# Kernel optimization log

Measured on AMD Instinct MI355X. Metric: run time of the kernel, lower is better.

Reference implementation:

```python
import jax, jax.numpy as jnp
import numpy as np

B, S, D = 2, 2048, 2048
H, DH = 16, 128  # heads, dhead


def setup_inputs() -> dict:
    key = jax.random.key(0)
    k1, k2, k3 = jax.random.split(key, 3)
    x = jax.random.normal(k1, (B, S, D), dtype=jnp.float32)
    # torch Linear weights: [out_features, in_features], fan_in-scaled init
    w_in = jax.random.normal(k2, (3 * H * DH, D), dtype=jnp.float32) * (1.0 / np.sqrt(D))
    w_out = jax.random.normal(k3, (D, H * DH), dtype=jnp.float32) * (1.0 / np.sqrt(H * DH))
    return {"x": x, "w_in": w_in, "w_out": w_out}


def reference(x, w_in, w_out):
    b, s, _ = x.shape
    # input projection (no bias): [b, s, 3*H*DH]
    projected = jnp.einsum("bsd,ed->bse", x, w_in)
    # view(b, s, H, 3*DH) then chunk along last dim -> q, k, v each [b, s, H, DH]
    projected = projected.reshape(b, s, H, 3 * DH)
    q, k, v = jnp.split(projected, 3, axis=-1)
    # naive path: scores [b, H, s, s]
    scores = jnp.einsum("bqhd,bkhd->bhqk", q, k) * (1.0 / np.sqrt(DH))
    # causal mask (tril keeps, upper triangle -> -inf)
    causal_mask = jnp.tril(jnp.ones((s, s), dtype=bool))
    scores = jnp.where(causal_mask, scores, jnp.float32(-jnp.inf))
    attn = jax.nn.softmax(scores, axis=-1)
    # PV: [b, s, H, DH]
    out = jnp.einsum("bhqk,bkhd->bqhd", attn, v)
    out = out.reshape(b, s, H * DH)
    # output projection (no bias): [b, s, D]
    return jnp.einsum("bse,de->bsd", out, w_out)
```

## Files before the change

kernel.cpp:

```cpp
#include <hip/hip_runtime.h>
#include <hip/hip_bf16.h>
#include <math.h>


typedef short bf16x8 __attribute__((ext_vector_type(8)));
typedef float f32x4 __attribute__((ext_vector_type(4)));

#define NEG_BIG -30000.0f

__device__ __forceinline__ short f2bf(float f) {
    union { float f; unsigned u; } v; v.f = f;
    unsigned r = v.u + 0x7fffu + ((v.u >> 16) & 1u);
    return (short)(r >> 16);
}

__device__ __forceinline__ int pack2bf(float a, float b) {
    return (int)((((unsigned)f2bf(b)) << 16) | (((unsigned)f2bf(a)) & 0xffffu));
}

#define GLDS16(g, l) \
    __builtin_amdgcn_global_load_lds((const __attribute__((address_space(1))) void*)(g), \
                                     (__attribute__((address_space(3))) void*)(l), 16, 0, 0)

__global__ __launch_bounds__(256) void cvt_f32_bf16(const float* __restrict__ src,
                                                    short* __restrict__ dst, int n) {
    int i = (blockIdx.x * blockDim.x + threadIdx.x) * 4;
    if (i < n) {
        float4 v = *(const float4*)(src + i);
        short4 o;
        o.x = f2bf(v.x); o.y = f2bf(v.y); o.z = f2bf(v.z); o.w = f2bf(v.w);
        *(short4*)(dst + i) = o;
    }
}

template <int BN, bool F32OUT>
__global__ __launch_bounds__(256) void gemm_bt(const short* __restrict__ A,
                                               const short* __restrict__ Bm,
                                               void* __restrict__ Cv,
                                               int N, int K) {
    constexpr int NT = BN / 32;
    constexpr int SUBA = 128 * 32;
    constexpr int SUBB = BN * 32;
    __shared__ short sA[2 * SUBA];
    __shared__ short sB[2 * SUBB];
    const int lane = threadIdx.x & 63;
    const int w = threadIdx.x >> 6;
    const int l15 = lane & 15, quad = lane >> 4;
    const int bm0 = blockIdx.y * 128, bn0 = blockIdx.x * BN;

    const int c1 = w * 64 + lane;
    const short* gA = A + (size_t)(bm0 + (c1 >> 2)) * K + (c1 & 3) * 8;
    const short* gB = Bm + (size_t)(bn0 + (c1 >> 2)) * K + (c1 & 3) * 8;
    const size_t half64 = (size_t)64 * K;
    short* lA1 = sA + w * 512;
    short* lA2 = sA + 2048 + w * 512;
    short* lB1 = sB + w * 512;
    short* lB2 = sB + 2048 + w * 512;

    const int wm = (w >> 1) * 64, wn = (w & 1) * (BN / 2);
    const short* pa = sA + (wm + l15) * 32 + quad * 8;
    const short* pb = sB + (wn + l15) * 32 + quad * 8;

    f32x4 acc[4][NT] = {};
    for (int k0 = 0; k0 < K; k0 += 64) {
        #pragma unroll
        for (int s = 0; s < 2; s++) {
            const int ks = k0 + s * 32;
            GLDS16(gA + ks, lA1 + s * SUBA);
            GLDS16(gA + half64 + ks, lA2 + s * SUBA);
            GLDS16(gB + ks, lB1 + s * SUBB);
            if constexpr (BN == 128) GLDS16(gB + half64 + ks, lB2 + s * SUBB);
        }
        __syncthreads();
        #pragma unroll
        for (int s = 0; s < 2; s++) {
            bf16x8 af[4], bf[NT];
            #pragma unroll
            for (int mt = 0; mt < 4; mt++) af[mt] = *(const bf16x8*)(pa + s * SUBA + mt * 512);
            #pragma unroll
            for (int nt = 0; nt < NT; nt++) bf[nt] = *(const bf16x8*)(pb + s * SUBB + nt * 512);
            #pragma unroll
            for (int mt = 0; mt < 4; mt++)
                #pragma unroll
                for (int nt = 0; nt < NT; nt++)
                    acc[mt][nt] = __builtin_amdgcn_mfma_f32_16x16x32_bf16(af[mt], bf[nt], acc[mt][nt], 0, 0, 0);
        }
        __syncthreads();
    }
    #pragma unroll
    for (int mt = 0; mt < 4; mt++)
        #pragma unroll
        for (int nt = 0; nt < NT; nt++)
            #pragma unroll
            for (int r = 0; r < 4; r++) {
                int row = bm0 + wm + mt * 16 + quad * 4 + r;
                int col = bn0 + wn + nt * 16 + l15;
                if (F32OUT)
                    ((float*)Cv)[(size_t)row * N + col] = acc[mt][nt][r];
                else
                    ((short*)Cv)[(size_t)row * N + col] = f2bf(acc[mt][nt][r]);
            }
}

#define VP 40
__global__ __launch_bounds__(512) void attn_kernel(const short* __restrict__ P,
                                                   short* __restrict__ O) {
    constexpr int S = 2048, ROWW = 6144, HD = 2048;
    const int id = blockIdx.x;
    const int b = id >> 8;
    const int rr = id & 255;
    const int h = rr & 15;
    const int t0 = rr >> 4;
    const int qt = b ? (15 - t0) : t0;
    const int wave = threadIdx.x >> 6, lane = threadIdx.x & 63;
    const int l15 = lane & 15, quad = lane >> 4;
    const int qRow = qt * 128 + wave * 16;
    const short* Pb = P + (size_t)b * S * ROWW;
    const short* Qp = Pb + h * 384;
    const short* Kp = Qp + 128;
    const short* Vp = Qp + 256;

    __shared__ short sK[2][32 * 128];
    __shared__ short sVt[2][128 * VP];

    bf16x8 qf[4];
    #pragma unroll
    for (int f = 0; f < 4; f++)
        qf[f] = *(const bf16x8*)(Qp + (size_t)(qRow + l15) * ROWW + f * 32 + quad * 8);

    const bool isK = wave < 4;
    const int c1 = (wave & 3) * 64 + lane;
    const int krow1 = c1 >> 4;
    const int kcol = ((c1 & 15) ^ (krow1 & 15)) * 8;
    const short* gK1 = Kp + (size_t)krow1 * ROWW + kcol;
    const short* gK2 = Kp + (size_t)(krow1 + 16) * ROWW + kcol;
    const int ldsOff1 = (wave & 3) * 512;
    const int ldsOff2 = 2048 + (wave & 3) * 512;
    const int vt = (int)threadIdx.x - 256;
    const int vKey = vt & 31;
    const int vD0 = (vt >> 5) * 8;
    const short* gV = Vp + (size_t)vKey * ROWW + vD0;

    const int kTiles = qt * 4 + 4;
    const float scale = 0.08838834764831845f;
    const int qG = qRow + l15;

    f32x4 accO[8] = {};
    float m_i = NEG_BIG, l_i = 0.f;

    if (isK) {
        GLDS16(gK1, &sK[0][ldsOff1]);
        GLDS16(gK2, &sK[0][ldsOff2]);
    } else {
        bf16x8 v0 = *(const bf16x8*)(gV);
        bf16x8 v1 = *(const bf16x8*)(gV + 64);
        #pragma unroll
        for (int j = 0; j < 8; j++) {
            sVt[0][(vD0 + j) * VP + vKey] = v0[j];
            sVt[0][(vD0 + 64 + j) * VP + vKey] = v1[j];
        }
    }
    __syncthreads();

    for (int kt = 0; kt < kTiles; kt++) {
        const int cur = kt & 1, nxt = cur ^ 1;
        const bool pre = (kt + 1 < kTiles);
        bf16x8 v0n, v1n;
        if (pre) {
            const size_t kOff = (size_t)(kt + 1) * 32 * ROWW;
            if (isK) {
                GLDS16(gK1 + kOff, &sK[nxt][ldsOff1]);
                GLDS16(gK2 + kOff, &sK[nxt][ldsOff2]);
            } else {
                v0n = *(const bf16x8*)(gV + kOff);
                v1n = *(const bf16x8*)(gV + kOff + 64);
            }
        }
        f32x4 sc[2] = {};
        #pragma unroll
        for (int hh = 0; hh < 2; hh++) {
            const int row = hh * 16 + l15;
            #pragma unroll
            for (int f = 0; f < 4; f++) {
                const int jj = (4 * f + quad) ^ l15;
                bf16x8 kf = *(const bf16x8*)(&sK[cur][row * 128 + jj * 8]);
                sc[hh] = __builtin_amdgcn_mfma_f32_16x16x32_bf16(kf, qf[f], sc[hh], 0, 0, 0);
            }
        }
        #pragma unroll
        for (int hh = 0; hh < 2; hh++)
            #pragma unroll
            for (int r = 0; r < 4; r++) {
                int key = kt * 32 + hh * 16 + quad * 4 + r;
                float v = sc[hh][r] * scale;
                sc[hh][r] = (key <= qG) ? v : NEG_BIG;
            }
        float mloc = sc[0][0];
        #pragma unroll
        for (int r = 1; r < 4; r++) mloc = fmaxf(mloc, sc[0][r]);
        #pragma unroll
        for (int r = 0; r < 4; r++) mloc = fmaxf(mloc, sc[1][r]);
        mloc = fmaxf(mloc, __shfl_xor(mloc, 16));
        mloc = fmaxf(mloc, __shfl_xor(mloc, 32));
        const float nm = fmaxf(m_i, mloc);
        const float alpha = __expf(m_i - nm);
        m_i = nm;
        float ssum = 0.f;
        #pragma unroll
        for (int hh = 0; hh < 2; hh++)
            #pragma unroll
            for (int r = 0; r < 4; r++) {
                float p = __expf(sc[hh][r] - nm);
                sc[hh][r] = p;
                ssum += p;
            }
        ssum += __shfl_xor(ssum, 16);
        ssum += __shfl_xor(ssum, 32);
        l_i = alpha * l_i + ssum;
        #pragma unroll
        for (int t = 0; t < 8; t++)
            #pragma unroll
            for (int r = 0; r < 4; r++) accO[t][r] *= alpha;
        const int d00 = pack2bf(sc[0][0], sc[0][1]);
        const int d01 = pack2bf(sc[0][2], sc[0][3]);
        const int d10 = pack2bf(sc[1][0], sc[1][1]);
        const int d11 = pack2bf(sc[1][2], sc[1][3]);
        const int srcA = l15 + ((quad & 1) << 5);
        const int srcB = srcA + 16;
        const int s00 = __shfl(d00, srcA), s01 = __shfl(d01, srcA);
        const int s02 = __shfl(d00, srcB), s03 = __shfl(d01, srcB);
        const int s10 = __shfl(d10, srcA), s11 = __shfl(d11, srcA);
        const int s12 = __shfl(d10, srcB), s13 = __shfl(d11, srcB);
        union { int i[4]; bf16x8 v; } pu;
        const bool lo = quad < 2;
        pu.i[0] = lo ? s00 : s10;
        pu.i[1] = lo ? s01 : s11;
        pu.i[2] = lo ? s02 : s12;
        pu.i[3] = lo ? s03 : s13;
        const bf16x8 pf = pu.v;
        #pragma unroll
        for (int t = 0; t < 8; t++) {
            bf16x8 vf = *(const bf16x8*)(&sVt[cur][(t * 16 + l15) * VP + quad * 8]);
            accO[t] = __builtin_amdgcn_mfma_f32_16x16x32_bf16(vf, pf, accO[t], 0, 0, 0);
        }
        if (pre && !isK) {
            #pragma unroll
            for (int j = 0; j < 8; j++) {
                sVt[nxt][(vD0 + j) * VP + vKey] = v0n[j];
                sVt[nxt][(vD0 + 64 + j) * VP + vKey] = v1n[j];
            }
        }
        __syncthreads();
    }
    const float inv = 1.0f / l_i;
    #pragma unroll
    for (int t = 0; t < 8; t++) {
        short4 st;
        st.x = f2bf(accO[t][0] * inv);
        st.y = f2bf(accO[t][1] * inv);
        st.z = f2bf(accO[t][2] * inv);
        st.w = f2bf(accO[t][3] * inv);
        *(short4*)(&O[(size_t)(b * S + qG) * HD + h * 128 + t * 16 + quad * 4]) = st;
    }
}

extern "C" void kernel_launch(void* const* d_in, const int* in_sizes, int n_in,
                              void* d_out, int out_size, void* d_ws, size_t ws_size,
                              hipStream_t stream) {
    const float* x     = (const float*)d_in[0];
    const float* w_in  = (const float*)d_in[1];
    const float* w_out = (const float*)d_in[2];
    float* out = (float*)d_out;

    short* Pbuf   = (short*)d_ws;
    short* xObuf  = Pbuf  + (size_t)4096 * 6144;
    short* winb   = xObuf + (size_t)8388608;
    short* woutb  = winb  + (size_t)6144 * 2048;

    dim3 blk(256, 1, 1);
    const int nx = 2 * 2048 * 2048, nwi = 6144 * 2048, nwo = 2048 * 2048;
    hipLaunchKernelGGL(cvt_f32_bf16, dim3(nx / 1024), blk, 0, stream, x, xObuf, nx);
    hipLaunchKernelGGL(cvt_f32_bf16, dim3(nwi / 1024), blk, 0, stream, w_in, winb, nwi);
    hipLaunchKernelGGL(cvt_f32_bf16, dim3(nwo / 1024), blk, 0, stream, w_out, woutb, nwo);
    hipLaunchKernelGGL((gemm_bt<128, false>), dim3(48, 32, 1), blk, 0, stream, xObuf, winb, (void*)Pbuf, 6144, 2048);
    hipLaunchKernelGGL(attn_kernel, dim3(512, 1, 1), dim3(512, 1, 1), 0, stream, Pbuf, xObuf);
    hipLaunchKernelGGL((gemm_bt<64, true>), dim3(32, 32, 1), blk, 0, stream, xObuf, woutb, (void*)out, 2048, 2048);
}
```

Before: 387.0 us.

## Replace input-projection GEMM with 256x256-tile double-buffered pipelined kernel

Adds a new GEMM kernel with 256x256 output tiles, 512 threads and 8 waves. It uses XOR-swizzled LDS layouts, direct global-to-LDS loads and a phased prefetch schedule that interleaves loads with MFMA work, plus blockIdx swizzling for cache locality. The kernel is used for the QKV input projection. The aim is higher data reuse per tile and better overlap of memory traffic with compute. The cost is heavy register and LDS use (128 KB of shared memory) and a hand-tuned wait/barrier schedule that is fragile.

```diff
diff --git a/kernel.cpp b/kernel.cpp
--- a/kernel.cpp
+++ b/kernel.cpp
@@ -96,6 +96,134 @@
                 int row = bm0 + wm + mt * 16 + quad * 4 + r;
                 int col = bn0 + wn + nt * 16 + l15;
                 if (F32OUT)
+                    ((float*)Cv)[(size_t)row * N + col] = acc[mt][nt][r];
+                else
+                    ((short*)Cv)[(size_t)row * N + col] = f2bf(acc[mt][nt][r]);
+            }
+}
+
+struct MainT { static constexpr bool value = false; };
+struct TailT { static constexpr bool value = true; };
+
+template <bool F32OUT>
+__global__ __launch_bounds__(512, 2) void gemm256(const short* __restrict__ A,
+                                                  const short* __restrict__ Bm,
+                                                  void* __restrict__ Cv,
+                                                  int N, int K, int MT) {
+    __shared__ short sA[2][256 * 64];
+    __shared__ short sB[2][256 * 64];
+    const int tid = threadIdx.x;
+    const int lane = tid & 63, w = tid >> 6;
+    const int l15 = lane & 15, quad = lane >> 4;
+    const int wm = w >> 2, wn = w & 3;
+
+    const int cpx = (int)gridDim.x >> 3;
+    const int swz = ((int)blockIdx.x & 7) * cpx + ((int)blockIdx.x >> 3);
+    const int bm0 = (swz % MT) * 256;
+    const int bn0 = (swz / MT) * 256;
+
+    const int rloc = w * 8 + (lane >> 3);
+    const int csw = ((lane & 7) ^ ((lane >> 3) & 7)) * 8;
+    const short* gA = A + (size_t)(bm0 + rloc) * K + csw;
+    const short* gB = Bm + (size_t)(bn0 + rloc) * K + csw;
+
+    auto stA = [&](int buf, int R0, int t) {
+        GLDS16(gA + (size_t)R0 * K + t * 64, &sA[buf][R0 * 64 + w * 512]);
+    };
+    auto stB = [&](int buf, int R0, int t) {
+        GLDS16(gB + (size_t)R0 * K + t * 64, &sB[buf][R0 * 64 + w * 512]);
+    };
+
+    const int sx = l15 & 7;
+    auto ldA = [&](int buf, int r0, int ks) -> bf16x8 {
+        const int off = (r0 + l15) * 128 + (((ks * 4 + quad) ^ sx) << 4);
+        return *(const bf16x8*)((const char*)&sA[buf][0] + off);
+    };
+    auto ldB = [&](int buf, int r0, int ks) -> bf16x8 {
+        const int off = (r0 + l15) * 128 + (((ks * 4 + quad) ^ sx) << 4);
+        return *(const bf16x8*)((const char*)&sB[buf][0] + off);
+    };
+
+    f32x4 acc[8][4] = {};
+    bf16x8 bfr[4][2];
+
+    stB(0, 0, 0); stB(0, 64, 0); stB(0, 128, 0); stB(0, 192, 0);
+    stA(0, 0, 0); stA(0, 128, 0); stA(0, 64, 0); stA(0, 192, 0);
+    stB(1, 0, 1); stB(1, 64, 1); stB(1, 128, 1); stB(1, 192, 1);
+    stA(1, 0, 1); stA(1, 128, 1);
+    asm volatile("s_waitcnt vmcnt(6)" ::: "memory");
+    __builtin_amdgcn_s_barrier();
+
+    auto iter = [&](auto TC, int t0) {
+        constexpr bool TAIL = decltype(TC)::value;
+        #pragma unroll
+        for (int tt = 0; tt < 2; ++tt) {
+            const int buf = tt;
+            #pragma unroll
+            for (int q = 0; q < 4; ++q) {
+                const int ph = tt * 4 + q;
+                bf16x8 afr[2][2];
+                if (q == 0) {
+                    #pragma unroll
+                    for (int nt = 0; nt < 4; ++nt)
+                        #pragma unroll
+                        for (int ks = 0; ks < 2; ++ks)
+                            bfr[nt][ks] = ldB(buf, wn * 64 + nt * 16, ks);
+                }
+                #pragma unroll
+                for (int mt = 0; mt < 2; ++mt)
+                    #pragma unroll
+                    for (int ks = 0; ks < 2; ++ks)
+                        afr[mt][ks] = ldA(buf, wm * 128 + q * 32 + mt * 16, ks);
+                if (ph == 0) { stA(1, 64, t0 + 1); stA(1, 192, t0 + 1); }
+                if constexpr (!TAIL) {
+                    if (ph == 1) { stB(0, 0, t0 + 2); stB(0, 64, t0 + 2); }
+                    if (ph == 2) { stB(0, 128, t0 + 2); stB(0, 192, t0 + 2); }
+                    if (ph == 3) { stA(0, 0, t0 + 2); stA(0, 128, t0 + 2); }
+                    if (ph == 4) { stA(0, 64, t0 + 2); stA(0, 192, t0 + 2); }
+                    if (ph == 5) { stB(1, 0, t0 + 3); stB(1, 64, t0 + 3); }
+                    if (ph == 6) { stB(1, 128, t0 + 3); stB(1, 192, t0 + 3); }
+                    if (ph == 7) { stA(1, 0, t0 + 3); stA(1, 128, t0 + 3); }
+                }
+                __builtin_amdgcn_s_barrier();
+                asm volatile("s_waitcnt lgkmcnt(0)" ::: "memory");
+                __builtin_amdgcn_sched_barrier(0);
+                __builtin_amdgcn_s_setprio(1);
+                #pragma unroll
+                for (int mt = 0; mt < 2; ++mt)
+                    #pragma unroll
+                    for (int nt = 0; nt < 4; ++nt)
+                        #pragma unroll
+                        for (int ks = 0; ks < 2; ++ks)
+                            acc[q * 2 + mt][nt] = __builtin_amdgcn_mfma_f32_16x16x32_bf16(
+                                afr[mt][ks], bfr[nt][ks], acc[q * 2 + mt][nt], 0, 0, 0);
+                __builtin_amdgcn_s_setprio(0);
+                if (q == 3) {
+                    if constexpr (TAIL) {
+                        if (tt == 0) asm volatile("s_waitcnt vmcnt(0)" ::: "memory");
+                    } else {
+                        asm volatile("s_waitcnt vmcnt(6)" ::: "memory");
+                    }
+                }
+                __builtin_amdgcn_s_barrier();
+            }
+        }
+    };
+
+    const int NTt = K >> 6;
+    int t0 = 0;
+    for (; t0 < NTt - 2; t0 += 2) iter(MainT{}, t0);
+    iter(TailT{}, t0);
+
+    #pragma unroll
+    for (int mt = 0; mt < 8; ++mt)
+        #pragma unroll
+        for (int nt = 0; nt < 4; ++nt)
+            #pragma unroll
+            for (int r = 0; r < 4; ++r) {
+                const int row = bm0 + wm * 128 + mt * 16 + quad * 4 + r;
+                const int col = bn0 + wn * 64 + nt * 16 + l15;
+                if constexpr (F32OUT)
                     ((float*)Cv)[(size_t)row * N + col] = acc[mt][nt][r];
                 else
                     ((short*)Cv)[(size_t)row * N + col] = f2bf(acc[mt][nt][r]);
@@ -282,7 +410,8 @@
     hipLaunchKernelGGL(cvt_f32_bf16, dim3(nx / 1024), blk, 0, stream, x, xObuf, nx);
     hipLaunchKernelGGL(cvt_f32_bf16, dim3(nwi / 1024), blk, 0, stream, w_in, winb, nwi);
     hipLaunchKernelGGL(cvt_f32_bf16, dim3(nwo / 1024), blk, 0, stream, w_out, woutb, nwo);
-    hipLaunchKernelGGL((gemm_bt<128, false>), dim3(48, 32, 1), blk, 0, stream, xObuf, winb, (void*)Pbuf, 6144, 2048);
+    hipLaunchKernelGGL((gemm256<false>), dim3(384, 1, 1), dim3(512, 1, 1), 0, stream,
+                       xObuf, winb, (void*)Pbuf, 6144, 2048, 16);
     hipLaunchKernelGGL(attn_kernel, dim3(512, 1, 1), dim3(512, 1, 1), 0, stream, Pbuf, xObuf);
     hipLaunchKernelGGL((gemm_bt<64, true>), dim3(32, 32, 1), blk, 0, stream, xObuf, woutb, (void*)out, 2048, 2048);
 }
```

After: 395.0 us. 2.1% more time.
